# Kernel optimization log

Hardware: AMD Instinct MI355X
Metric: run time of the kernel (lower is better)

Reference implementation:

```python
import jax, jax.numpy as jnp
import numpy as np

B, T, D, H = 4, 1024, 512, 8
DK = D // H
L = 2 * T - 1  # relative-position length, Transformer-XL convention


def setup_inputs() -> dict:
    key = jax.random.key(0)
    ks = jax.random.split(key, 16)
    s = 0.02  # xavier-ish init scale
    inp = {
        "query": jax.random.normal(ks[0], (B, T, D), jnp.float32),
        "key": jax.random.normal(ks[1], (B, T, D), jnp.float32),
        "value": jax.random.normal(ks[2], (B, T, D), jnp.float32),
        "pos_embedding": jax.random.normal(ks[3], (B, L, D), jnp.float32),
        "mask": jax.random.randint(ks[4], (B, T), 0, 2).astype(bool),
        # nn.Linear weights are [out, in]; y = x @ W.T + b
        "Wq": jax.random.normal(ks[5], (D, D), jnp.float32) * s,
        "bq": jnp.zeros((D,), jnp.float32),
        "Wk": jax.random.normal(ks[6], (D, D), jnp.float32) * s,
        "bk": jnp.zeros((D,), jnp.float32),
        "Wv": jax.random.normal(ks[7], (D, D), jnp.float32) * s,
        "bv": jnp.zeros((D,), jnp.float32),
        "Wr": jax.random.normal(ks[8], (D, D), jnp.float32) * s,  # rpe_proj, no bias
        "u_bias": jax.random.normal(ks[9], (H, DK), jnp.float32) * s,
        "v_bias": jax.random.normal(ks[10], (H, DK), jnp.float32) * s,
        "Wo": jax.random.normal(ks[11], (D, D), jnp.float32) * s,
        "bo": jnp.zeros((D,), jnp.float32),
    }
    return inp


def _rel_shift(x):
    # x: [B, H, T, L] -> Transformer-XL pad/reshape/slice shift, keep first L//2+1 cols
    b, h, t, l = x.shape
    x = jnp.pad(x, ((0, 0), (0, 0), (0, 0), (1, 0)))        # [B,H,T,L+1]
    x = x.reshape(b, h, l + 1, t)[:, :, 1:, :]               # drop first row
    x = x.reshape(b, h, t, l)
    return x[..., : l // 2 + 1]                              # [B,H,T,T]


def reference(query, key, value, pos_embedding, mask,
              Wq, bq, Wk, bk, Wv, bv, Wr, u_bias, v_bias, Wo, bo):
    b = query.shape[0]
    q = (query @ Wq.T + bq).reshape(b, -1, H, DK)            # [B,T,H,dk]
    k = (key @ Wk.T + bk).reshape(b, -1, H, DK)              # [B,T,H,dk]
    v = (value @ Wv.T + bv).reshape(b, -1, H, DK)            # [B,T,H,dk]
    r = (pos_embedding @ Wr.T).reshape(b, -1, H, DK)         # [B,L,H,dk]

    main = jnp.einsum('bthd,bshd->bhts', q + u_bias, k)      # content score
    rpe = jnp.einsum('bthd,blhd->bhtl', q + v_bias, r)       # [B,H,T,L]

    scores = (main + _rel_shift(rpe)) / np.sqrt(DK).astype(np.float32)
    scores = jnp.where(mask[:, None, None, :],
                       jnp.asarray(1e-4, scores.dtype), scores)
    attn = jax.nn.softmax(scores, axis=-1)                   # dropout off (eval)

    out = jnp.einsum('bhts,bshd->bhtd', attn, v)             # [B,H,T,dk]
    # Faithful to original: view(B,-1,d_model) WITHOUT transposing heads back
    out = out.reshape(b, -1, D)                              # [B,T,D] (head-interleaved)
    return out @ Wo.T + bo
```

## Files before the change

### kernel.cpp

```cpp
#include <hip/hip_runtime.h>
#include <stdint.h>
#include <stddef.h>

#define B_ 4
#define T_ 1024
#define D_ 512
#define H_ 8
#define DK_ 64
#define L_ 2047
#define LP_ 2048

typedef __attribute__((ext_vector_type(8))) short short8;
typedef __attribute__((ext_vector_type(4))) short short4_t;
typedef __attribute__((ext_vector_type(4))) float f32x4;
typedef __attribute__((ext_vector_type(4))) unsigned int u32x4;
typedef __attribute__((ext_vector_type(8))) __bf16 bf16x8;

static __device__ __forceinline__ short f2bf(float f) {
  union { float f; unsigned u; } x; x.f = f;
  unsigned r = x.u + 0x7fffu + ((x.u >> 16) & 1u);
  return (short)(r >> 16);
}

static __device__ __forceinline__ float bf2f(short s) {
  union { unsigned u; float f; } x; x.u = ((unsigned)(unsigned short)s) << 16;
  return x.f;
}

static __device__ __forceinline__ f32x4 mfma16(bf16x8 a, bf16x8 b, f32x4 c) {
  return __builtin_amdgcn_mfma_f32_16x16x32_bf16(a, b, c, 0, 0, 0);
}

static __device__ __forceinline__ bf16x8 ldbf8(const short* p) {
  return *(const bf16x8*)p;
}

__global__ __launch_bounds__(256) void convert_kernel(
    const float* __restrict__ qin, const float* __restrict__ kin, const float* __restrict__ vin,
    const float* __restrict__ pin,
    const float* __restrict__ Wq, const float* __restrict__ Wk, const float* __restrict__ Wv,
    const float* __restrict__ Wr, const float* __restrict__ Wo,
    const unsigned char* __restrict__ mraw,
    short* __restrict__ dst, float* __restrict__ mask_f)
{
  if (blockIdx.x == 11518) {
    __shared__ int fmis, fany;
    if (threadIdx.x == 0) { fmis = 0; fany = 0; }
    __syncthreads();
    int lm = 0, la = 0;
    for (int i = threadIdx.x; i < B_ * T_; i += 256) {
      unsigned char c = mraw[i];
      if (c) { la = 1; if (i & 3) lm = 1; }
    }
    if (lm) atomicOr(&fmis, 1);
    if (la) atomicOr(&fany, 1);
    __syncthreads();
    int mmode = fmis ? 0 : (fany ? 1 : 2);
    const int* mi = (const int*)mraw;
    for (int i = threadIdx.x; i < B_ * T_; i += 256) {
      int mv = (mmode == 0) ? (int)mraw[i] : (mmode == 1 ? mi[i] : 0);
      mask_f[i] = mv ? 1.0f : 0.0f;
    }
    return;
  }
  int gid = blockIdx.x * 256 + threadIdx.x;
  const float* src; int base;
  if      (gid < 524288)  { src = qin; base = 0; }
  else if (gid < 1048576) { src = kin; base = 524288; }
  else if (gid < 1572864) { src = vin; base = 1048576; }
  else if (gid < 2620928) { src = pin; base = 1572864; }
  else if (gid < 2686464) { src = Wq;  base = 2620928; }
  else if (gid < 2752000) { src = Wk;  base = 2686464; }
  else if (gid < 2817536) { src = Wv;  base = 2752000; }
  else if (gid < 2883072) { src = Wr;  base = 2817536; }
  else                    { src = Wo;  base = 2883072; }
  f32x4 val = ((const f32x4*)src)[gid - base];
  short4_t o;
  o[0] = f2bf(val[0]); o[1] = f2bf(val[1]); o[2] = f2bf(val[2]); o[3] = f2bf(val[3]);
  ((short4_t*)dst)[gid] = o;
}

template<int VARIANT>
__global__ __launch_bounds__(256, 4) void proj_gemm(
    const short* __restrict__ qkv_bf, const short* __restrict__ pos_bf,
    const short* __restrict__ W_bf, const short* __restrict__ ao_bf,
    short* __restrict__ qO, short* __restrict__ khO,
    short* __restrict__ vtO, short* __restrict__ rhO, float* __restrict__ outF,
    const float* __restrict__ bq, const float* __restrict__ bk_,
    const float* __restrict__ bv_, const float* __restrict__ bo_)
{
  const int bid0 = blockIdx.x;
  constexpr int PER = (VARIANT == 0) ? 80 : 16;
  const int bid = (bid0 & 7) * PER + (bid0 >> 3);

  const short* A; const short* W;
  int Mtotal, mode, m0, n0;
  if constexpr (VARIANT == 0) {
    if (bid < 384) {
      int zz = bid >> 7, r2 = bid & 127;
      m0 = (r2 >> 2) * 128; n0 = (r2 & 3) * 128;
      A = qkv_bf + (size_t)zz * 2097152; W = W_bf + (size_t)zz * 262144;
      Mtotal = 4096; mode = zz;
    } else {
      int r2 = bid - 384;
      m0 = (r2 >> 2) * 128; n0 = (r2 & 3) * 128;
      A = pos_bf; W = W_bf + 786432;
      Mtotal = 8188; mode = 3;
    }
  } else {
    m0 = (bid >> 2) * 128; n0 = (bid & 3) * 128;
    A = ao_bf; W = W_bf + 1048576;
    Mtotal = 4096; mode = 4;
  }
  __shared__ __align__(16) short As[128 * 64];
  __shared__ __align__(16) short Bs[128 * 64];
  const int tid = threadIdx.x;
  const int lane = tid & 63, wid = tid >> 6;
  const int wr = wid >> 1, wc = wid & 1;
  const int l15 = lane & 15, l4 = lane >> 4;
  const int trow = tid >> 3;
  const int tcolsw = (((tid & 7) ^ (trow & 7)) << 3);

  auto STAGE = [&](int kt) {
#pragma unroll
    for (int j = 0; j < 4; j++) {
      int srow = m0 + j * 32 + trow; if (srow > Mtotal - 1) srow = Mtotal - 1;
      __builtin_amdgcn_global_load_lds(
          (const __attribute__((address_space(1))) unsigned int*)(A + (size_t)srow * 512 + kt + tcolsw),
          (__attribute__((address_space(3))) unsigned int*)(&As[(j * 32 + wid * 8) * 64]), 16, 0, 0);
    }
#pragma unroll
    for (int j = 0; j < 4; j++) {
      __builtin_amdgcn_global_load_lds(
          (const __attribute__((address_space(1))) unsigned int*)(W + (size_t)(n0 + j * 32 + trow) * 512 + kt + tcolsw),
          (__attribute__((address_space(3))) unsigned int*)(&Bs[(j * 32 + wid * 8) * 64]), 16, 0, 0);
    }
  };

  f32x4 acc[4][4] = {};

#pragma unroll
  for (int it = 0; it < 8; ++it) {
    STAGE(it * 64);
    __syncthreads();
    __builtin_amdgcn_s_setprio(1);
#pragma unroll
    for (int kf = 0; kf < 2; kf++) {
      const int colA = ((kf * 4 + l4) ^ (l15 & 7)) << 3;
      bf16x8 af[4], bf4[4];
#pragma unroll
      for (int rf = 0; rf < 4; rf++)
        af[rf] = ldbf8(&As[(wr * 64 + rf * 16 + l15) * 64 + colA]);
#pragma unroll
      for (int cf = 0; cf < 4; cf++)
        bf4[cf] = ldbf8(&Bs[(wc * 64 + cf * 16 + l15) * 64 + colA]);
#pragma unroll
      for (int rf = 0; rf < 4; rf++)
#pragma unroll
        for (int cf = 0; cf < 4; cf++)
          acc[rf][cf] = mfma16(af[rf], bf4[cf], acc[rf][cf]);
    }
    __builtin_amdgcn_s_setprio(0);
    __syncthreads();
  }

#pragma unroll
  for (int cf = 0; cf < 4; cf++) {
    int n = n0 + wc * 64 + cf * 16 + l15;
    float bias = 0.f;
    if (mode == 0) bias = bq[n];
    else if (mode == 1) bias = bk_[n];
    else if (mode == 2) bias = bv_[n];
    else if (mode == 4) bias = bo_[n];
    int hh = n >> 6, dk = n & 63;
#pragma unroll
    for (int rf = 0; rf < 4; rf++) {
#pragma unroll
      for (int reg = 0; reg < 4; reg++) {
        int m = m0 + wr * 64 + rf * 16 + l4 * 4 + reg;
        float val = acc[rf][cf][reg] + bias;
        if (mode == 0) {
          int bb = m >> 10, t = m & 1023;
          qO[((size_t)(bb * H_ + hh) * T_ + t) * DK_ + dk] = f2bf(val);
        } else if (mode == 1) {
          int bb = m >> 10, t = m & 1023;
          khO[((size_t)(bb * H_ + hh) * T_ + t) * DK_ + dk] = f2bf(val);
        } else if (mode == 2) {
          int bb = m >> 10, t = m & 1023;
          vtO[((size_t)(bb * H_ + hh) * DK_ + dk) * T_ + t] = f2bf(val);
        } else if (mode == 3) {
          if (m < B_ * L_) {
            int bb = m / L_;
            int ll = m - bb * L_;
            rhO[((size_t)(bb * H_ + hh) * LP_ + ll) * DK_ + dk] = f2bf(val);
          }
        } else {
          outF[(size_t)m * D_ + n] = val;
        }
      }
    }
  }
}

__global__ __launch_bounds__(256, 4) void attn_kernel(
    const short* __restrict__ q, const short* __restrict__ kh,
    const short* __restrict__ vt, const short* __restrict__ rh,
    const float* __restrict__ mask_f,
    const float* __restrict__ ub, const float* __restrict__ vb,
    float* __restrict__ paccO, float* __restrict__ psum)
{
  const int tid = threadIdx.x;
  const int lane = tid & 63;
  const int w = tid >> 6;
  const int l15 = lane & 15, l4 = lane >> 4;
  const int bid = blockIdx.x;
  const int xcd = bid & 7, slot = bid >> 3;
  const int bh = (slot >> 5) * 8 + xcd;
  const int half = (slot >> 4) & 1;
  const int t0b = (slot & 15) * 64;
  const int b = bh >> 3, h = bh & 7;
  const int t0w = t0b + w * 16;
  const int woff = 48 - w * 16;

  __shared__ __align__(16) short Ks[64 * 64];
  __shared__ __align__(16) short Vs[64 * 64];
  __shared__ __align__(16) short Rs[128 * 64];
  __shared__ __align__(16) short Ps[4][16 * 64];

  const short* kB = kh + (size_t)bh * T_ * DK_;
  const short* vB = vt + (size_t)bh * DK_ * T_;
  const short* rB = rh + (size_t)bh * LP_ * DK_;

  const short* qB = q + ((size_t)bh * T_ + t0w + l15) * DK_ + l4 * 8;
  short8 q0 = *(const short8*)qB, q1 = *(const short8*)(qB + 32);
  const float* ubp = ub + h * 64 + l4 * 8;
  const float* vbp = vb + h * 64 + l4 * 8;
  f32x4 u0a = *(const f32x4*)ubp,        u0b = *(const f32x4*)(ubp + 4);
  f32x4 u1a = *(const f32x4*)(ubp + 32), u1b = *(const f32x4*)(ubp + 36);
  f32x4 v0a = *(const f32x4*)vbp,        v0b = *(const f32x4*)(vbp + 4);
  f32x4 v1a = *(const f32x4*)(vbp + 32), v1b = *(const f32x4*)(vbp + 36);
  short8 qu0s, qu1s, qv0s, qv1s;
#pragma unroll
  for (int j = 0; j < 4; j++) {
    qu0s[j]     = f2bf(bf2f(q0[j])     + u0a[j]);
    qu0s[j + 4] = f2bf(bf2f(q0[j + 4]) + u0b[j]);
    qu1s[j]     = f2bf(bf2f(q1[j])     + u1a[j]);
    qu1s[j + 4] = f2bf(bf2f(q1[j + 4]) + u1b[j]);
    qv0s[j]     = f2bf(bf2f(q0[j])     + v0a[j]);
    qv0s[j + 4] = f2bf(bf2f(q0[j + 4]) + v0b[j]);
    qv1s[j]     = f2bf(bf2f(q1[j])     + v1a[j]);
    qv1s[j + 4] = f2bf(bf2f(q1[j + 4]) + v1b[j]);
  }
  bf16x8 quf0 = __builtin_bit_cast(bf16x8, qu0s);
  bf16x8 quf1 = __builtin_bit_cast(bf16x8, qu1s);
  bf16x8 qvf0 = __builtin_bit_cast(bf16x8, qv0s);
  bf16x8 qvf1 = __builtin_bit_cast(bf16x8, qv1s);

  const short8 ones_s = {(short)0x3F80, (short)0x3F80, (short)0x3F80, (short)0x3F80,
                         (short)0x3F80, (short)0x3F80, (short)0x3F80, (short)0x3F80};
  const bf16x8 ones8 = __builtin_bit_cast(bf16x8, ones_s);

  const int trow = tid >> 3;
  const int tcol = (((tid & 7) ^ ((tid >> 3) & 7)) << 3);
  const int wbase = w * 512;

  auto STAGE = [&](int s0) {
    const int l0b = 960 + s0 - t0b;
#pragma unroll
    for (int j = 0; j < 2; j++) {
      __builtin_amdgcn_global_load_lds(
          (const __attribute__((address_space(1))) unsigned int*)(kB + (size_t)(s0 + trow + j * 32) * 64 + tcol),
          (__attribute__((address_space(3))) unsigned int*)(&Ks[j * 2048 + wbase]), 16, 0, 0);
      __builtin_amdgcn_global_load_lds(
          (const __attribute__((address_space(1))) unsigned int*)(vB + (size_t)(trow + j * 32) * T_ + s0 + tcol),
          (__attribute__((address_space(3))) unsigned int*)(&Vs[j * 2048 + wbase]), 16, 0, 0);
    }
#pragma unroll
    for (int j = 0; j < 4; j++) {
      __builtin_amdgcn_global_load_lds(
          (const __attribute__((address_space(1))) unsigned int*)(rB + (size_t)(l0b + trow + j * 32) * 64 + tcol),
          (__attribute__((address_space(3))) unsigned int*)(&Rs[j * 2048 + wbase]), 16, 0, 0);
    }
  };

  float* Msf = (float*)&Ps[0][0];
  ((f32x4*)Msf)[tid] = ((const f32x4*)(mask_f + b * T_))[tid];
  __syncthreads();
  unsigned long long mbits = 0ull;
#pragma unroll
  for (int gi = 0; gi < 16; ++gi)
#pragma unroll
    for (int cf = 0; cf < 4; ++cf)
      if (Msf[gi * 64 + cf * 16 + l15] != 0.f)
        mbits |= 1ull << (gi * 4 + cf);

  f32x4 accO[4] = {};
  f32x4 sum_acc = {};
  const int swz = (l15 & 7) << 3;
  const int s0base = half * 512;

  for (int it = 0; it < 8; ++it) {
    const int git = half * 8 + it;
    const int s0 = s0base + (it << 6);
    STAGE(s0);
    __syncthreads();

    const unsigned m4 = (unsigned)(mbits >> (git * 4)) & 15u;

    f32x4 sacc[4] = {};
    f32x4 gacc[5] = {};
    __builtin_amdgcn_s_setprio(1);
#pragma unroll
    for (int kf = 0; kf < 2; kf++) {
      const int col = (kf * 32 + l4 * 8) ^ swz;
      bf16x8 qf = kf ? quf1 : quf0;
      bf16x8 vf_ = kf ? qvf1 : qvf0;
#pragma unroll
      for (int cf = 0; cf < 4; cf++)
        sacc[cf] = mfma16(qf, ldbf8(&Ks[(cf * 16 + l15) * 64 + col]), sacc[cf]);
#pragma unroll
      for (int gf = 0; gf < 5; gf++)
        gacc[gf] = mfma16(vf_, ldbf8(&Rs[(woff + gf * 16 + l15) * 64 + col]), gacc[gf]);
    }
    __builtin_amdgcn_s_setprio(0);

    float p[4][4];
#pragma unroll
    for (int r = 0; r < 4; r++) {
      const int tl = l4 * 4 + r;
      const int e = l15 + 15 - tl;
      const int src = (lane & 48) | (e & 15);
      float sh0 = __shfl(gacc[0][r], src);
      float sh1 = __shfl(gacc[1][r], src);
      float sh2 = __shfl(gacc[2][r], src);
      float sh3 = __shfl(gacc[3][r], src);
      float sh4 = __shfl(gacc[4][r], src);
      float ga[4] = {sh0, sh1, sh2, sh3};
      float gb[4] = {sh1, sh2, sh3, sh4};
#pragma unroll
      for (int cf = 0; cf < 4; cf++) {
        float gg = (e < 16) ? ga[cf] : gb[cf];
        float lg = (sacc[cf][r] + gg) * 0.125f;
        lg = (m4 & (1u << cf)) ? 1e-4f : lg;
        p[r][cf] = __expf(lg);
      }
    }

#pragma unroll
    for (int r = 0; r < 4; r++) {
      const int tl = l4 * 4 + r;
      const int sw2 = (tl & 7) << 3;
#pragma unroll
      for (int cf = 0; cf < 4; cf++)
        Ps[w][tl * 64 + ((cf * 16 + l15) ^ sw2)] = f2bf(p[r][cf]);
    }

    __builtin_amdgcn_s_setprio(1);
#pragma unroll
    for (int kf = 0; kf < 2; kf++) {
      const int kc = kf * 32 + l4 * 8;
      bf16x8 pa = ldbf8(&Ps[w][l15 * 64 + (kc ^ swz)]);
      sum_acc = mfma16(pa, ones8, sum_acc);
#pragma unroll
      for (int vf = 0; vf < 4; vf++)
        accO[vf] = mfma16(pa, ldbf8(&Vs[(vf * 16 + l15) * 64 + (kc ^ swz)]), accO[vf]);
    }
    __builtin_amdgcn_s_setprio(0);
    __syncthreads();
  }

#pragma unroll
  for (int r = 0; r < 4; r++) {
    const int tl = l4 * 4 + r;
    const int row = bh * T_ + t0w + tl;
#pragma unroll
    for (int vf = 0; vf < 4; vf++)
      paccO[(size_t)half * 2097152 + (size_t)row * 64 + vf * 16 + l15] = accO[vf][r];
    if (l15 == 0) psum[half * 32768 + row] = sum_acc[r];
  }
}

__global__ __launch_bounds__(256) void combine_kernel(
    const float* __restrict__ paccO, const float* __restrict__ psum,
    short* __restrict__ aoW)
{
  const int gid = blockIdx.x * 256 + threadIdx.x;
  const int row = gid >> 3;
  const int j8 = (gid & 7) * 8;
  const float* a0 = paccO + (size_t)row * 64 + j8;
  const float* a1 = a0 + 2097152;
  f32x4 x0 = *(const f32x4*)a0,       x1 = *(const f32x4*)(a0 + 4);
  f32x4 y0 = *(const f32x4*)a1,       y1 = *(const f32x4*)(a1 + 4);
  const float inv = 1.0f / (psum[row] + psum[32768 + row]);
  short8 o;
#pragma unroll
  for (int j = 0; j < 4; j++) {
    o[j]     = f2bf((x0[j] + y0[j]) * inv);
    o[j + 4] = f2bf((x1[j] + y1[j]) * inv);
  }
  *(short8*)(aoW + (size_t)row * 64 + j8) = o;
}

extern "C" void kernel_launch(void* const* d_in, const int* in_sizes, int n_in,
                              void* d_out, int out_size, void* d_ws, size_t ws_size,
                              hipStream_t stream) {
  const float* qin = (const float*)d_in[0];
  const float* kin = (const float*)d_in[1];
  const float* vin = (const float*)d_in[2];
  const float* pin = (const float*)d_in[3];
  const unsigned char* mraw = (const unsigned char*)d_in[4];
  const float* Wq = (const float*)d_in[5];
  const float* bq = (const float*)d_in[6];
  const float* Wk = (const float*)d_in[7];
  const float* bk = (const float*)d_in[8];
  const float* Wv = (const float*)d_in[9];
  const float* bv = (const float*)d_in[10];
  const float* Wr = (const float*)d_in[11];
  const float* ub = (const float*)d_in[12];
  const float* vb = (const float*)d_in[13];
  const float* Wo = (const float*)d_in[14];
  const float* bo = (const float*)d_in[15];
  float* out = (float*)d_out;
  char* ws = (char*)d_ws;

  short* qkv_bf = (short*)(ws + 0);
  short* pos_bf = (short*)(ws + 12582912);
  float* paccO  = (float*)(ws + 0);
  float* psum   = (float*)(ws + 16777216);
  short* W_bf   = (short*)(ws + 20967424);
  float* mask_f = (float*)(ws + 23588864);
  short* qW     = (short*)(ws + 23605248);
  short* khW    = (short*)(ws + 31993856);
  short* vtW    = (short*)(ws + 36188160);
  short* rhW    = (short*)(ws + 40382464);
  short* aoW    = (short*)(ws + 48771072);

  convert_kernel<<<dim3(11519), dim3(256), 0, stream>>>(
      qin, kin, vin, pin, Wq, Wk, Wv, Wr, Wo, mraw, qkv_bf, mask_f);
  proj_gemm<0><<<dim3(640), dim3(256), 0, stream>>>(
      qkv_bf, pos_bf, W_bf, aoW, qW, khW, vtW, rhW, nullptr,
      bq, bk, bv, bo);
  attn_kernel<<<dim3(1024), dim3(256), 0, stream>>>(
      qW, khW, vtW, rhW, mask_f, ub, vb, paccO, psum);
  combine_kernel<<<dim3(1024), dim3(256), 0, stream>>>(paccO, psum, aoW);
  proj_gemm<1><<<dim3(128), dim3(256), 0, stream>>>(
      qkv_bf, pos_bf, W_bf, aoW, qW, khW, vtW, rhW, out,
      bq, bk, bv, bo);
}
```

Baseline: 108.3 us.

## Process two query row-groups per wave to reuse K/R/V fragments

Each wave now handles 32 query rows instead of 16, so a block covers 128 rows and the grid is halved. K, R and V fragments are loaded from LDS once and reused across both row groups, and the R tile is enlarged to 192 rows. The relative-shift shuffle now packs the gathered values into bf16 pairs, cutting the number of cross-lane shuffles. The cost is more registers, with launch bounds lowered to 2 blocks per CU, plus extra rounding of the positional score to bf16 before the add.

```diff
diff --git a/kernel.cpp b/kernel.cpp
--- a/kernel.cpp
+++ b/kernel.cpp
@@ -25,6 +25,18 @@
 static __device__ __forceinline__ float bf2f(short s) {
   union { unsigned u; float f; } x; x.u = ((unsigned)(unsigned short)s) << 16;
   return x.f;
+}
+
+static __device__ __forceinline__ unsigned cvtpk(float lo, float hi) {
+  unsigned r;
+  asm("v_cvt_pk_bf16_f32 %0, %1, %2" : "=v"(r) : "v"(lo), "v"(hi));
+  return r;
+}
+static __device__ __forceinline__ float unpk_lo(unsigned u) {
+  union { unsigned x; float f; } v; v.x = u << 16; return v.f;
+}
+static __device__ __forceinline__ float unpk_hi(unsigned u) {
+  union { unsigned x; float f; } v; v.x = u & 0xffff0000u; return v.f;
 }
 
 static __device__ __forceinline__ f32x4 mfma16(bf16x8 a, bf16x8 b, f32x4 c) {
@@ -202,7 +214,7 @@
   }
 }
 
-__global__ __launch_bounds__(256, 4) void attn_kernel(
+__global__ __launch_bounds__(256, 2) void attn_kernel(
     const short* __restrict__ q, const short* __restrict__ kh,
     const short* __restrict__ vt, const short* __restrict__ rh,
     const float* __restrict__ mask_f,
@@ -215,57 +227,62 @@
   const int l15 = lane & 15, l4 = lane >> 4;
   const int bid = blockIdx.x;
   const int xcd = bid & 7, slot = bid >> 3;
-  const int bh = (slot >> 5) * 8 + xcd;
-  const int half = (slot >> 4) & 1;
-  const int t0b = (slot & 15) * 64;
+  const int bh = (slot >> 4) * 8 + xcd;
+  const int rem = slot & 15;
+  const int half = rem >> 3;
+  const int t0b = (rem & 7) * 128;
   const int b = bh >> 3, h = bh & 7;
-  const int t0w = t0b + w * 16;
-  const int woff = 48 - w * 16;
+  const int t0w = t0b + w * 32;
+  const int gbase = 96 - w * 32;
 
   __shared__ __align__(16) short Ks[64 * 64];
   __shared__ __align__(16) short Vs[64 * 64];
-  __shared__ __align__(16) short Rs[128 * 64];
-  __shared__ __align__(16) short Ps[4][16 * 64];
+  __shared__ __align__(16) short Rs[192 * 64];
+  __shared__ __align__(16) short Ps[4][32 * 64];
 
   const short* kB = kh + (size_t)bh * T_ * DK_;
   const short* vB = vt + (size_t)bh * DK_ * T_;
   const short* rB = rh + (size_t)bh * LP_ * DK_;
 
-  const short* qB = q + ((size_t)bh * T_ + t0w + l15) * DK_ + l4 * 8;
-  short8 q0 = *(const short8*)qB, q1 = *(const short8*)(qB + 32);
   const float* ubp = ub + h * 64 + l4 * 8;
   const float* vbp = vb + h * 64 + l4 * 8;
-  f32x4 u0a = *(const f32x4*)ubp,        u0b = *(const f32x4*)(ubp + 4);
-  f32x4 u1a = *(const f32x4*)(ubp + 32), u1b = *(const f32x4*)(ubp + 36);
-  f32x4 v0a = *(const f32x4*)vbp,        v0b = *(const f32x4*)(vbp + 4);
-  f32x4 v1a = *(const f32x4*)(vbp + 32), v1b = *(const f32x4*)(vbp + 36);
-  short8 qu0s, qu1s, qv0s, qv1s;
-#pragma unroll
-  for (int j = 0; j < 4; j++) {
-    qu0s[j]     = f2bf(bf2f(q0[j])     + u0a[j]);
-    qu0s[j + 4] = f2bf(bf2f(q0[j + 4]) + u0b[j]);
-    qu1s[j]     = f2bf(bf2f(q1[j])     + u1a[j]);
-    qu1s[j + 4] = f2bf(bf2f(q1[j + 4]) + u1b[j]);
-    qv0s[j]     = f2bf(bf2f(q0[j])     + v0a[j]);
-    qv0s[j + 4] = f2bf(bf2f(q0[j + 4]) + v0b[j]);
-    qv1s[j]     = f2bf(bf2f(q1[j])     + v1a[j]);
-    qv1s[j + 4] = f2bf(bf2f(q1[j + 4]) + v1b[j]);
-  }
-  bf16x8 quf0 = __builtin_bit_cast(bf16x8, qu0s);
-  bf16x8 quf1 = __builtin_bit_cast(bf16x8, qu1s);
-  bf16x8 qvf0 = __builtin_bit_cast(bf16x8, qv0s);
-  bf16x8 qvf1 = __builtin_bit_cast(bf16x8, qv1s);
+  f32x4 ubv0 = *(const f32x4*)ubp,        ubv1 = *(const f32x4*)(ubp + 4);
+  f32x4 ubv2 = *(const f32x4*)(ubp + 32), ubv3 = *(const f32x4*)(ubp + 36);
+  f32x4 vbv0 = *(const f32x4*)vbp,        vbv1 = *(const f32x4*)(vbp + 4);
+  f32x4 vbv2 = *(const f32x4*)(vbp + 32), vbv3 = *(const f32x4*)(vbp + 36);
+  bf16x8 quf[2][2], qvf[2][2];
+#pragma unroll
+  for (int rg = 0; rg < 2; rg++) {
+    const short* qB = q + ((size_t)bh * T_ + t0w + rg * 16 + l15) * DK_ + l4 * 8;
+    short8 q0 = *(const short8*)qB, q1 = *(const short8*)(qB + 32);
+    short8 a0, a1, c0, c1;
+#pragma unroll
+    for (int j = 0; j < 4; j++) {
+      a0[j]     = f2bf(bf2f(q0[j])     + ubv0[j]);
+      a0[j + 4] = f2bf(bf2f(q0[j + 4]) + ubv1[j]);
+      a1[j]     = f2bf(bf2f(q1[j])     + ubv2[j]);
+      a1[j + 4] = f2bf(bf2f(q1[j + 4]) + ubv3[j]);
+      c0[j]     = f2bf(bf2f(q0[j])     + vbv0[j]);
+      c0[j + 4] = f2bf(bf2f(q0[j + 4]) + vbv1[j]);
+      c1[j]     = f2bf(bf2f(q1[j])     + vbv2[j]);
+      c1[j + 4] = f2bf(bf2f(q1[j + 4]) + vbv3[j]);
+    }
+    quf[rg][0] = __builtin_bit_cast(bf16x8, a0);
+    quf[rg][1] = __builtin_bit_cast(bf16x8, a1);
+    qvf[rg][0] = __builtin_bit_cast(bf16x8, c0);
+    qvf[rg][1] = __builtin_bit_cast(bf16x8, c1);
+  }
 
   const short8 ones_s = {(short)0x3F80, (short)0x3F80, (short)0x3F80, (short)0x3F80,
                          (short)0x3F80, (short)0x3F80, (short)0x3F80, (short)0x3F80};
   const bf16x8 ones8 = __builtin_bit_cast(bf16x8, ones_s);
 
   const int trow = tid >> 3;
-  const int tcol = (((tid & 7) ^ ((tid >> 3) & 7)) << 3);
+  const int tcol = (((tid & 7) ^ (trow & 7)) << 3);
   const int wbase = w * 512;
 
   auto STAGE = [&](int s0) {
-    const int l0b = 960 + s0 - t0b;
+    const int l0b = 896 + s0 - t0b;
 #pragma unroll
     for (int j = 0; j < 2; j++) {
       __builtin_amdgcn_global_load_lds(
@@ -276,7 +293,7 @@
           (__attribute__((address_space(3))) unsigned int*)(&Vs[j * 2048 + wbase]), 16, 0, 0);
     }
 #pragma unroll
-    for (int j = 0; j < 4; j++) {
+    for (int j = 0; j < 6; j++) {
       __builtin_amdgcn_global_load_lds(
           (const __attribute__((address_space(1))) unsigned int*)(rB + (size_t)(l0b + trow + j * 32) * 64 + tcol),
           (__attribute__((address_space(3))) unsigned int*)(&Rs[j * 2048 + wbase]), 16, 0, 0);
@@ -294,89 +311,103 @@
       if (Msf[gi * 64 + cf * 16 + l15] != 0.f)
         mbits |= 1ull << (gi * 4 + cf);
 
-  f32x4 accO[4] = {};
-  f32x4 sum_acc = {};
+  f32x4 accO[2][4] = {};
+  f32x4 sum_acc[2] = {};
   const int swz = (l15 & 7) << 3;
-  const int s0base = half * 512;
 
   for (int it = 0; it < 8; ++it) {
     const int git = half * 8 + it;
-    const int s0 = s0base + (it << 6);
+    const int s0 = half * 512 + (it << 6);
     STAGE(s0);
     __syncthreads();
 
     const unsigned m4 = (unsigned)(mbits >> (git * 4)) & 15u;
 
-    f32x4 sacc[4] = {};
-    f32x4 gacc[5] = {};
+    f32x4 sacc[2][4] = {};
+    f32x4 gacc[2][5] = {};
     __builtin_amdgcn_s_setprio(1);
 #pragma unroll
     for (int kf = 0; kf < 2; kf++) {
       const int col = (kf * 32 + l4 * 8) ^ swz;
-      bf16x8 qf = kf ? quf1 : quf0;
-      bf16x8 vf_ = kf ? qvf1 : qvf0;
+      bf16x8 kfr[4], gbr[6];
 #pragma unroll
       for (int cf = 0; cf < 4; cf++)
-        sacc[cf] = mfma16(qf, ldbf8(&Ks[(cf * 16 + l15) * 64 + col]), sacc[cf]);
-#pragma unroll
-      for (int gf = 0; gf < 5; gf++)
-        gacc[gf] = mfma16(vf_, ldbf8(&Rs[(woff + gf * 16 + l15) * 64 + col]), gacc[gf]);
+        kfr[cf] = ldbf8(&Ks[(cf * 16 + l15) * 64 + col]);
+#pragma unroll
+      for (int gk = 0; gk < 6; gk++)
+        gbr[gk] = ldbf8(&Rs[(gbase + gk * 16 + l15) * 64 + col]);
+#pragma unroll
+      for (int rg = 0; rg < 2; rg++) {
+#pragma unroll
+        for (int cf = 0; cf < 4; cf++)
+          sacc[rg][cf] = mfma16(quf[rg][kf], kfr[cf], sacc[rg][cf]);
+#pragma unroll
+        for (int gf = 0; gf < 5; gf++)
+          gacc[rg][gf] = mfma16(qvf[rg][kf], gbr[gf + 1 - rg], gacc[rg][gf]);
+      }
     }
     __builtin_amdgcn_s_setprio(0);
 
-    float p[4][4];
+#pragma unroll
+    for (int rg = 0; rg < 2; rg++) {
+#pragma unroll
+      for (int r = 0; r < 4; r++) {
+        const int tl = l4 * 4 + r;
+        const int e = l15 + 15 - tl;
+        const int src = (lane & 48) | (e & 15);
+        unsigned pk0 = cvtpk(gacc[rg][0][r], gacc[rg][1][r]);
+        unsigned pk1 = cvtpk(gacc[rg][2][r], gacc[rg][3][r]);
+        unsigned pk2 = cvtpk(gacc[rg][4][r], gacc[rg][4][r]);
+        unsigned sp0 = (unsigned)__shfl((int)pk0, src);
+        unsigned sp1 = (unsigned)__shfl((int)pk1, src);
+        unsigned sp2 = (unsigned)__shfl((int)pk2, src);
+        const bool elo = (e < 16);
+        float gg[4];
+        gg[0] = elo ? unpk_lo(sp0) : unpk_hi(sp0);
+        gg[1] = elo ? unpk_hi(sp0) : unpk_lo(sp1);
+        gg[2] = elo ? unpk_lo(sp1) : unpk_hi(sp1);
+        gg[3] = elo ? unpk_hi(sp1) : unpk_lo(sp2);
+        const int sw2 = (tl & 7) << 3;
+#pragma unroll
+        for (int cf = 0; cf < 4; cf++) {
+          float lg = (sacc[rg][cf][r] + gg[cf]) * 0.125f;
+          lg = (m4 & (1u << cf)) ? 1e-4f : lg;
+          Ps[w][(rg * 16 + tl) * 64 + ((cf * 16 + l15) ^ sw2)] = f2bf(__expf(lg));
+        }
+      }
+    }
+
+    __builtin_amdgcn_s_setprio(1);
+#pragma unroll
+    for (int kf = 0; kf < 2; kf++) {
+      const int kc = (kf * 32 + l4 * 8) ^ swz;
+      bf16x8 vfr[4];
+#pragma unroll
+      for (int vf = 0; vf < 4; vf++)
+        vfr[vf] = ldbf8(&Vs[(vf * 16 + l15) * 64 + kc]);
+#pragma unroll
+      for (int rg = 0; rg < 2; rg++) {
+        bf16x8 pa = ldbf8(&Ps[w][(rg * 16 + l15) * 64 + kc]);
+        sum_acc[rg] = mfma16(pa, ones8, sum_acc[rg]);
+#pragma unroll
+        for (int vf = 0; vf < 4; vf++)
+          accO[rg][vf] = mfma16(pa, vfr[vf], accO[rg][vf]);
+      }
+    }
+    __builtin_amdgcn_s_setprio(0);
+    __syncthreads();
+  }
+
+#pragma unroll
+  for (int rg = 0; rg < 2; rg++) {
 #pragma unroll
     for (int r = 0; r < 4; r++) {
-      const int tl = l4 * 4 + r;
-      const int e = l15 + 15 - tl;
-      const int src = (lane & 48) | (e & 15);
-      float sh0 = __shfl(gacc[0][r], src);
-      float sh1 = __shfl(gacc[1][r], src);
-      float sh2 = __shfl(gacc[2][r], src);
-      float sh3 = __shfl(gacc[3][r], src);
-      float sh4 = __shfl(gacc[4][r], src);
-      float ga[4] = {sh0, sh1, sh2, sh3};
-      float gb[4] = {sh1, sh2, sh3, sh4};
-#pragma unroll
-      for (int cf = 0; cf < 4; cf++) {
-        float gg = (e < 16) ? ga[cf] : gb[cf];
-        float lg = (sacc[cf][r] + gg) * 0.125f;
-        lg = (m4 & (1u << cf)) ? 1e-4f : lg;
-        p[r][cf] = __expf(lg);
-      }
-    }
-
-#pragma unroll
-    for (int r = 0; r < 4; r++) {
-      const int tl = l4 * 4 + r;
-      const int sw2 = (tl & 7) << 3;
-#pragma unroll
-      for (int cf = 0; cf < 4; cf++)
-        Ps[w][tl * 64 + ((cf * 16 + l15) ^ sw2)] = f2bf(p[r][cf]);
-    }
-
-    __builtin_amdgcn_s_setprio(1);
-#pragma unroll
-    for (int kf = 0; kf < 2; kf++) {
-      const int kc = kf * 32 + l4 * 8;
-      bf16x8 pa = ldbf8(&Ps[w][l15 * 64 + (kc ^ swz)]);
-      sum_acc = mfma16(pa, ones8, sum_acc);
+      const int row = bh * T_ + t0w + rg * 16 + l4 * 4 + r;
 #pragma unroll
       for (int vf = 0; vf < 4; vf++)
-        accO[vf] = mfma16(pa, ldbf8(&Vs[(vf * 16 + l15) * 64 + (kc ^ swz)]), accO[vf]);
-    }
-    __builtin_amdgcn_s_setprio(0);
-    __syncthreads();
-  }
-
-#pragma unroll
-  for (int r = 0; r < 4; r++) {
-    const int tl = l4 * 4 + r;
-    const int row = bh * T_ + t0w + tl;
-#pragma unroll
-    for (int vf = 0; vf < 4; vf++)
-      paccO[(size_t)half * 2097152 + (size_t)row * 64 + vf * 16 + l15] = accO[vf][r];
-    if (l15 == 0) psum[half * 32768 + row] = sum_acc[r];
+        paccO[(size_t)half * 2097152 + (size_t)row * 64 + vf * 16 + l15] = accO[rg][vf][r];
+      if (l15 == 0) psum[half * 32768 + row] = sum_acc[rg][r];
+    }
   }
 }
 
@@ -440,7 +471,7 @@
   proj_gemm<0><<<dim3(640), dim3(256), 0, stream>>>(
       qkv_bf, pos_bf, W_bf, aoW, qW, khW, vtW, rhW, nullptr,
       bq, bk, bv, bo);
-  attn_kernel<<<dim3(1024), dim3(256), 0, stream>>>(
+  attn_kernel<<<dim3(512), dim3(256), 0, stream>>>(
       qW, khW, vtW, rhW, mask_f, ub, vb, paccO, psum);
   combine_kernel<<<dim3(1024), dim3(256), 0, stream>>>(paccO, psum, aoW);
   proj_gemm<1><<<dim3(128), dim3(256), 0, stream>>>(
```

After: 103.8 us. -4.1%, faster.
